# Optimization experiments

Measured on AMD Instinct MI355X. Metric: run time of the kernel, lower is better.

Reference implementation:

```python
import jax, jax.numpy as jnp
import numpy as np

B, C_IN, C_OUT, H, MAXN = 128, 32, 32, 4096, 6


def setup_inputs() -> dict:
    key = jax.random.key(0)
    ks = jax.random.split(key, 6)
    x = jax.random.normal(ks[0], (B, C_IN, H), dtype=jnp.float32)
    weight = jax.random.normal(ks[1], (C_OUT, C_IN, MAXN + 1), dtype=jnp.float32) * 0.05
    bias = jax.random.normal(ks[2], (C_OUT,), dtype=jnp.float32) * 0.05
    gamma = jnp.ones((C_OUT,), dtype=jnp.float32)
    beta = jnp.zeros((C_OUT,), dtype=jnp.float32)
    # hex neighbor table; -1 marks invalid (boundary) neighbors
    neighbors = jax.random.randint(ks[3], (H, MAXN), -1, H, dtype=jnp.int64)
    return {"x": x, "weight": weight, "bias": bias, "gamma": gamma,
            "beta": beta, "neighbors": neighbors, "groups": 1}


def reference(x, weight, bias, gamma, beta, neighbors, groups):
    Bsz, Cin, Hn = x.shape
    Cout, _, K = weight.shape  # K = total_inputs = max_neighbors + 1
    G = groups
    # global std normalization (torch std: unbiased, ddof=1)
    x = x / (jnp.std(x, ddof=1) + 1e-5)
    valid = (neighbors >= 0)                      # [H, K-1]
    idx = jnp.clip(neighbors, 0, None)
    nbr = x[:, :, idx] * valid.astype(x.dtype)[None, None]   # [B,C,H,K-1]
    allv = jnp.concatenate([x[..., None], nbr], axis=3)      # [B,C,H,K]
    allv = allv.reshape(Bsz, G, Cin // G, Hn, K)
    w = weight.reshape(G, Cout // G, Cin // G, K)
    out = jnp.einsum('bgihk,goik->bgoh', allv, w).reshape(Bsz, Cout, Hn)
    total_valid = valid.sum(axis=1).astype(out.dtype)[None, None] + 1.0  # [1,1,H]
    out = out / (total_valid + 1e-6)
    out = out + bias[None, :, None]
    # BatchNorm1d in training mode: per-channel over (batch, hex), biased var
    mean = out.mean(axis=(0, 2), keepdims=True)
    var = out.var(axis=(0, 2), keepdims=True)
    out = gamma[None, :, None] * (out - mean) * jax.lax.rsqrt(var + 1e-5) + beta[None, :, None]
    return out
```

## Files before the change

### kernel.cpp

```cpp
#include <hip/hip_runtime.h>
#include <stdint.h>
#include <stddef.h>

#define BSZ 128
#define CIN 32
#define COUT 32
#define HN 4096
#define K7 7
#define NTOT (BSZ*CIN*HN)
#define NBH  (BSZ*HN)

typedef __attribute__((ext_vector_type(8))) short short8;
typedef __attribute__((ext_vector_type(4))) float f32x4;

#define WS_OB   0
#define WS_WT   33554432
#define WS_NBR  33568768
#define WS_INVD 33699840
#define WS_OSTP 33716224
#define WS_OST  33781760

__device__ __forceinline__ unsigned short f32_to_bf16(float f){
    union { float f; uint32_t u; } v; v.f = f;
    uint32_t u = v.u;
    return (unsigned short)((u + 0x7FFFu + ((u >> 16) & 1u)) >> 16);
}
__device__ __forceinline__ float bf16_to_f32(unsigned short h){
    union { uint32_t u; float f; } v; v.u = ((uint32_t)h) << 16;
    return v.f;
}

__global__ void kinit(const int* __restrict__ nbr,
                      const float* __restrict__ w,
                      int* __restrict__ nbr_pack,
                      float* __restrict__ invd,
                      unsigned short* __restrict__ wt,
                      float* __restrict__ ostatp){
    int t = threadIdx.x;
    if (blockIdx.x < 16){
        int h = blockIdx.x*256 + t;
        #pragma unroll
        for (int j = 0; j < 4; j++) ostatp[h*4 + j] = 0.0f;
        int cnt = 0;
        int pk[8];
        #pragma unroll
        for (int j = 0; j < 6; j++){
            int iv = nbr[h*6 + j];
            if (iv >= HN) iv = HN - 1;
            if (iv >= 0) cnt++; else iv = -1;
            pk[j] = iv;
        }
        pk[6] = cnt; pk[7] = 0;
        #pragma unroll
        for (int j = 0; j < 8; j++) nbr_pack[h*8 + j] = pk[j];
        invd[h] = 1.0f / ((float)cnt + 1.0f + 1e-6f);
    } else {
        for (int i = t; i < COUT*K7*CIN; i += 256){
            int o  = i / (K7*CIN);
            int kk = (i / CIN) % K7;
            int c  = i % CIN;
            wt[i] = f32_to_bf16(w[(o*CIN + c)*K7 + kk]);
        }
    }
}

__global__ void ktrans(const float* __restrict__ x,
                       unsigned short* __restrict__ xt){
    __shared__ float tile[32][260];
    int b  = blockIdx.x >> 4;
    int h0 = (blockIdx.x & 15) << 8;
    int t  = threadIdx.x;
    #pragma unroll
    for (int l = 0; l < 8; l++){
        int linear = l*256 + t;
        int c  = linear >> 6;
        int h4 = linear & 63;
        float4 v = *(const float4*)(x + ((size_t)(b*CIN + c))*HN + h0 + h4*4);
        *(float4*)&tile[c][h4*4] = v;
    }
    __syncthreads();
    int cg = (t & 3) * 8;
    int hw = t >> 2;
    #pragma unroll
    for (int r = 0; r < 4; r++){
        int h = r*64 + hw;
        alignas(16) unsigned short tmp[8];
        #pragma unroll
        for (int j = 0; j < 8; j++) tmp[j] = f32_to_bf16(tile[cg + j][h]);
        *(uint4*)(xt + ((size_t)(b*HN + h0 + h))*32 + cg) = *(const uint4*)tmp;
    }
}

__global__ __launch_bounds__(256) void kconv(
    const unsigned short* __restrict__ xt,
    const unsigned short* __restrict__ wt,
    const int* __restrict__ nbrp,
    const float* __restrict__ invd,
    unsigned short* __restrict__ ob,
    float* __restrict__ ostatp)
{
    int lane = threadIdx.x & 63;
    int wv   = threadIdx.x >> 6;
    int n    = lane & 15;
    int quad = lane >> 4;
    int xcd  = blockIdx.x & 7;
    int j    = blockIdx.x >> 3;
    int b    = xcd*16 + (j >> 4);
    int hbase= ((j & 15)*4 + wv) * 64;

    short8 af[2][K7];
    #pragma unroll
    for (int mt = 0; mt < 2; mt++){
        int o = n + 16*mt;
        #pragma unroll
        for (int kk = 0; kk < K7; kk++)
            af[mt][kk] = *(const short8*)(wt + (size_t)(o*K7 + kk)*CIN + quad*8);
    }

    float sacc[8]  = {0,0,0,0,0,0,0,0};
    float sacc2[8] = {0,0,0,0,0,0,0,0};
    const short8 zero8 = {0,0,0,0,0,0,0,0};
    const unsigned short* xb = xt + (size_t)b*HN*CIN;

    int h = hbase + n;
    int4 na = *(const int4*)(nbrp + h*8);
    int4 nb = *(const int4*)(nbrp + h*8 + 4);
    float idv = invd[h];

    #pragma unroll 1
    for (int it = 0; it < 4; it++){
        int hc = hbase + it*16 + n;
        int hn = hbase + (it < 3 ? it+1 : it)*16 + n;
        int4 na2 = *(const int4*)(nbrp + hn*8);
        int4 nb2 = *(const int4*)(nbrp + hn*8 + 4);
        float idv2 = invd[hn];

        short8 bfr[K7];
        bfr[0] = *(const short8*)(xb + (size_t)hc*CIN + quad*8);
        int rows[6] = {na.x, na.y, na.z, na.w, nb.x, nb.y};
        #pragma unroll
        for (int kk = 0; kk < 6; kk++){
            int row  = rows[kk];
            int rowc = row < 0 ? 0 : row;
            bfr[kk+1] = *(const short8*)(xb + (size_t)rowc*CIN + quad*8);
            if (row < 0) bfr[kk+1] = zero8;
        }
        f32x4 acc0 = {0.f,0.f,0.f,0.f};
        f32x4 acc1 = {0.f,0.f,0.f,0.f};
        #pragma unroll
        for (int kk = 0; kk < K7; kk++){
            acc0 = __builtin_amdgcn_mfma_f32_16x16x32_bf16(af[0][kk], bfr[kk], acc0, 0, 0, 0);
            acc1 = __builtin_amdgcn_mfma_f32_16x16x32_bf16(af[1][kk], bfr[kk], acc1, 0, 0, 0);
        }
        #pragma unroll
        for (int mt = 0; mt < 2; mt++){
            f32x4 a = mt ? acc1 : acc0;
            #pragma unroll
            for (int r = 0; r < 4; r++){
                int o = mt*16 + quad*4 + r;
                float v = a[r]*idv;
                ob[((size_t)(b*COUT + o))*HN + hc] = f32_to_bf16(v);
                sacc[mt*4 + r]  += v;
                sacc2[mt*4 + r] += v*v;
            }
        }
        na = na2; nb = nb2; idv = idv2;
    }
    #pragma unroll
    for (int bit = 1; bit < 16; bit <<= 1){
        #pragma unroll
        for (int i = 0; i < 8; i++){
            sacc[i]  += __shfl_xor(sacc[i],  bit);
            sacc2[i] += __shfl_xor(sacc2[i], bit);
        }
    }
    if (n == 0){
        int slot = blockIdx.x & 255;
        #pragma unroll
        for (int mt = 0; mt < 2; mt++)
            #pragma unroll
            for (int r = 0; r < 4; r++){
                int o = mt*16 + quad*4 + r;
                atomicAdd(&ostatp[slot*64 + o],      sacc[mt*4 + r]);
                atomicAdd(&ostatp[slot*64 + 32 + o], sacc2[mt*4 + r]);
            }
    }
}

__global__ void kred(const float* __restrict__ ostatp,
                     float* __restrict__ ostat){
    __shared__ float part[4][64];
    int t = threadIdx.x;
    int a = t & 63;
    int g = t >> 6;
    float s = 0.0f;
    #pragma unroll
    for (int j = 0; j < 64; j++)
        s += ostatp[(g*64 + j)*64 + a];
    part[g][a] = s;
    __syncthreads();
    if (t < 64)
        ostat[t] = part[0][t] + part[1][t] + part[2][t] + part[3][t];
}

__global__ void kbn(const unsigned short* __restrict__ ob,
                    float* __restrict__ out,
                    const float* __restrict__ ostat,
                    const float* __restrict__ gamma,
                    const float* __restrict__ beta){
    __shared__ float sc[32], sh[32];
    int t = threadIdx.x;
    if (t < 32){
        float mean = ostat[t] * (1.0f/(float)NBH);
        float var  = ostat[32 + t] * (1.0f/(float)NBH) - mean*mean;
        float s = gamma[t] * rsqrtf(var + 1e-5f);
        sc[t] = s;
        sh[t] = beta[t] - mean*s;
    }
    __syncthreads();
    int gid    = blockIdx.x*blockDim.x + t;
    int stride = gridDim.x*blockDim.x;
    for (int i = gid; i < NTOT/8; i += stride){
        int o = (i >> 9) & 31;
        uint4 raw = ((const uint4*)ob)[i];
        const unsigned short* p = (const unsigned short*)&raw;
        float s = sc[o], bsh = sh[o];
        float4 r0, r1;
        r0.x = bf16_to_f32(p[0])*s + bsh;
        r0.y = bf16_to_f32(p[1])*s + bsh;
        r0.z = bf16_to_f32(p[2])*s + bsh;
        r0.w = bf16_to_f32(p[3])*s + bsh;
        r1.x = bf16_to_f32(p[4])*s + bsh;
        r1.y = bf16_to_f32(p[5])*s + bsh;
        r1.z = bf16_to_f32(p[6])*s + bsh;
        r1.w = bf16_to_f32(p[7])*s + bsh;
        ((float4*)out)[i*2]     = r0;
        ((float4*)out)[i*2 + 1] = r1;
    }
}

extern "C" void kernel_launch(void* const* d_in, const int* in_sizes, int n_in,
                              void* d_out, int out_size, void* d_ws, size_t ws_size,
                              hipStream_t stream) {
    const float* x      = (const float*)d_in[0];
    const float* weight = (const float*)d_in[1];
    const float* gamma  = (const float*)d_in[3];
    const float* beta   = (const float*)d_in[4];
    const int*   nbr    = (const int*)d_in[5];

    char* ws = (char*)d_ws;
    unsigned short* ob    = (unsigned short*)(ws + WS_OB);
    unsigned short* wt    = (unsigned short*)(ws + WS_WT);
    int*            nbrp  = (int*)(ws + WS_NBR);
    float*          invd  = (float*)(ws + WS_INVD);
    float*          ostatp= (float*)(ws + WS_OSTP);
    float*          ostat = (float*)(ws + WS_OST);
    float*          out   = (float*)d_out;
    unsigned short* xt    = (unsigned short*)d_out + 16777216;

    kinit <<<17,   256, 0, stream>>>(nbr, weight, nbrp, invd, wt, ostatp);
    ktrans<<<2048, 256, 0, stream>>>(x, xt);
    kconv <<<2048, 256, 0, stream>>>(xt, wt, nbrp, invd, ob, ostatp);
    kred  <<<1,    256, 0, stream>>>(ostatp, ostat);
    kbn   <<<2048, 256, 0, stream>>>(ob, out, ostat, gamma, beta);
}
```

Measured before the change: 184.9 us.

## Recompute convolution in second pass to fuse BatchNorm apply and drop intermediate

Replaces the bf16 intermediate buffer and separate BN-apply kernel with a templated conv kernel run twice: once to accumulate channel statistics, once to recompute the conv and write normalized fp32 output directly. Also double-buffers the neighbor gathers and fully unrolls the hex loop to overlap loads with MFMA work. This trades extra conv compute and an extra read of the transposed input for removing the intermediate write/read, at the cost of higher register usage.

```diff
diff --git a/kernel.cpp b/kernel.cpp
--- a/kernel.cpp
+++ b/kernel.cpp
@@ -13,7 +13,7 @@
 typedef __attribute__((ext_vector_type(8))) short short8;
 typedef __attribute__((ext_vector_type(4))) float f32x4;
 
-#define WS_OB   0
+#define WS_XT   0
 #define WS_WT   33554432
 #define WS_NBR  33568768
 #define WS_INVD 33699840
@@ -24,10 +24,6 @@
     union { float f; uint32_t u; } v; v.f = f;
     uint32_t u = v.u;
     return (unsigned short)((u + 0x7FFFu + ((u >> 16) & 1u)) >> 16);
-}
-__device__ __forceinline__ float bf16_to_f32(unsigned short h){
-    union { uint32_t u; float f; } v; v.u = ((uint32_t)h) << 16;
-    return v.f;
 }
 
 __global__ void kinit(const int* __restrict__ nbr,
@@ -91,12 +87,30 @@
     }
 }
 
-__global__ __launch_bounds__(256) void kconv(
+__device__ __forceinline__ void gather7(short8* dst, const unsigned short* xb,
+                                        int selfrow, int4 na, int4 nb, int quad){
+    const short8 zero8 = {0,0,0,0,0,0,0,0};
+    dst[0] = *(const short8*)(xb + (size_t)selfrow*CIN + quad*8);
+    int rows[6] = {na.x, na.y, na.z, na.w, nb.x, nb.y};
+    #pragma unroll
+    for (int k = 0; k < 6; k++){
+        int r  = rows[k];
+        int rc = r < 0 ? 0 : r;
+        dst[k+1] = *(const short8*)(xb + (size_t)rc*CIN + quad*8);
+        if (r < 0) dst[k+1] = zero8;
+    }
+}
+
+template<bool APPLY>
+__global__ __launch_bounds__(256) void kconv_t(
     const unsigned short* __restrict__ xt,
     const unsigned short* __restrict__ wt,
     const int* __restrict__ nbrp,
     const float* __restrict__ invd,
-    unsigned short* __restrict__ ob,
+    const float* __restrict__ ostat,
+    const float* __restrict__ gamma,
+    const float* __restrict__ beta,
+    float* __restrict__ out,
     float* __restrict__ ostatp)
 {
     int lane = threadIdx.x & 63;
@@ -117,73 +131,92 @@
             af[mt][kk] = *(const short8*)(wt + (size_t)(o*K7 + kk)*CIN + quad*8);
     }
 
+    float sc8[2][4], sh8[2][4];
+    if (APPLY){
+        #pragma unroll
+        for (int mt = 0; mt < 2; mt++)
+            #pragma unroll
+            for (int r = 0; r < 4; r++){
+                int o = mt*16 + quad*4 + r;
+                float mean = ostat[o]      * (1.0f/(float)NBH);
+                float var  = ostat[32 + o] * (1.0f/(float)NBH) - mean*mean;
+                float s = gamma[o] * rsqrtf(var + 1e-5f);
+                sc8[mt][r] = s;
+                sh8[mt][r] = beta[o] - mean*s;
+            }
+    }
+
     float sacc[8]  = {0,0,0,0,0,0,0,0};
     float sacc2[8] = {0,0,0,0,0,0,0,0};
-    const short8 zero8 = {0,0,0,0,0,0,0,0};
     const unsigned short* xb = xt + (size_t)b*HN*CIN;
-
-    int h = hbase + n;
-    int4 na = *(const int4*)(nbrp + h*8);
-    int4 nb = *(const int4*)(nbrp + h*8 + 4);
-    float idv = invd[h];
-
-    #pragma unroll 1
+    int hn0 = hbase + n;
+
+    int4 na[2], nb[2]; float iv[2];
+    short8 buf[2][K7];
+    na[0] = *(const int4*)(nbrp + hn0*8);
+    nb[0] = *(const int4*)(nbrp + hn0*8 + 4);
+    iv[0] = invd[hn0];
+    na[1] = *(const int4*)(nbrp + (hn0+16)*8);
+    nb[1] = *(const int4*)(nbrp + (hn0+16)*8 + 4);
+    iv[1] = invd[hn0+16];
+    gather7(buf[0], xb, hn0, na[0], nb[0], quad);
+
+    #pragma unroll
     for (int it = 0; it < 4; it++){
-        int hc = hbase + it*16 + n;
-        int hn = hbase + (it < 3 ? it+1 : it)*16 + n;
-        int4 na2 = *(const int4*)(nbrp + hn*8);
-        int4 nb2 = *(const int4*)(nbrp + hn*8 + 4);
-        float idv2 = invd[hn];
-
-        short8 bfr[K7];
-        bfr[0] = *(const short8*)(xb + (size_t)hc*CIN + quad*8);
-        int rows[6] = {na.x, na.y, na.z, na.w, nb.x, nb.y};
-        #pragma unroll
-        for (int kk = 0; kk < 6; kk++){
-            int row  = rows[kk];
-            int rowc = row < 0 ? 0 : row;
-            bfr[kk+1] = *(const short8*)(xb + (size_t)rowc*CIN + quad*8);
-            if (row < 0) bfr[kk+1] = zero8;
+        int s = it & 1, o2 = s ^ 1;
+        float idv = iv[s];
+        if (it + 1 < 4)
+            gather7(buf[o2], xb, hn0 + (it+1)*16, na[o2], nb[o2], quad);
+        if (it + 2 < 4){
+            na[s] = *(const int4*)(nbrp + (hn0 + (it+2)*16)*8);
+            nb[s] = *(const int4*)(nbrp + (hn0 + (it+2)*16)*8 + 4);
+            iv[s] = invd[hn0 + (it+2)*16];
         }
         f32x4 acc0 = {0.f,0.f,0.f,0.f};
         f32x4 acc1 = {0.f,0.f,0.f,0.f};
         #pragma unroll
         for (int kk = 0; kk < K7; kk++){
-            acc0 = __builtin_amdgcn_mfma_f32_16x16x32_bf16(af[0][kk], bfr[kk], acc0, 0, 0, 0);
-            acc1 = __builtin_amdgcn_mfma_f32_16x16x32_bf16(af[1][kk], bfr[kk], acc1, 0, 0, 0);
-        }
+            acc0 = __builtin_amdgcn_mfma_f32_16x16x32_bf16(af[0][kk], buf[s][kk], acc0, 0, 0, 0);
+            acc1 = __builtin_amdgcn_mfma_f32_16x16x32_bf16(af[1][kk], buf[s][kk], acc1, 0, 0, 0);
+        }
+        int hc = hbase + it*16 + n;
         #pragma unroll
         for (int mt = 0; mt < 2; mt++){
             f32x4 a = mt ? acc1 : acc0;
             #pragma unroll
             for (int r = 0; r < 4; r++){
-                int o = mt*16 + quad*4 + r;
                 float v = a[r]*idv;
-                ob[((size_t)(b*COUT + o))*HN + hc] = f32_to_bf16(v);
-                sacc[mt*4 + r]  += v;
-                sacc2[mt*4 + r] += v*v;
+                if (APPLY){
+                    int o = mt*16 + quad*4 + r;
+                    out[((size_t)(b*COUT + o))*HN + hc] = v*sc8[mt][r] + sh8[mt][r];
+                } else {
+                    sacc[mt*4 + r]  += v;
+                    sacc2[mt*4 + r] += v*v;
+                }
             }
         }
-        na = na2; nb = nb2; idv = idv2;
-    }
-    #pragma unroll
-    for (int bit = 1; bit < 16; bit <<= 1){
-        #pragma unroll
-        for (int i = 0; i < 8; i++){
-            sacc[i]  += __shfl_xor(sacc[i],  bit);
-            sacc2[i] += __shfl_xor(sacc2[i], bit);
-        }
-    }
-    if (n == 0){
-        int slot = blockIdx.x & 255;
-        #pragma unroll
-        for (int mt = 0; mt < 2; mt++)
-            #pragma unroll
-            for (int r = 0; r < 4; r++){
-                int o = mt*16 + quad*4 + r;
-                atomicAdd(&ostatp[slot*64 + o],      sacc[mt*4 + r]);
-                atomicAdd(&ostatp[slot*64 + 32 + o], sacc2[mt*4 + r]);
+    }
+
+    if (!APPLY){
+        #pragma unroll
+        for (int bit = 1; bit < 16; bit <<= 1){
+            #pragma unroll
+            for (int i = 0; i < 8; i++){
+                sacc[i]  += __shfl_xor(sacc[i],  bit);
+                sacc2[i] += __shfl_xor(sacc2[i], bit);
             }
+        }
+        if (n == 0){
+            int slot = blockIdx.x & 255;
+            #pragma unroll
+            for (int mt = 0; mt < 2; mt++)
+                #pragma unroll
+                for (int r = 0; r < 4; r++){
+                    int o = mt*16 + quad*4 + r;
+                    atomicAdd(&ostatp[slot*64 + o],      sacc[mt*4 + r]);
+                    atomicAdd(&ostatp[slot*64 + 32 + o], sacc2[mt*4 + r]);
+                }
+        }
     }
 }
 
@@ -201,42 +234,6 @@
     __syncthreads();
     if (t < 64)
         ostat[t] = part[0][t] + part[1][t] + part[2][t] + part[3][t];
-}
-
-__global__ void kbn(const unsigned short* __restrict__ ob,
-                    float* __restrict__ out,
-                    const float* __restrict__ ostat,
-                    const float* __restrict__ gamma,
-                    const float* __restrict__ beta){
-    __shared__ float sc[32], sh[32];
-    int t = threadIdx.x;
-    if (t < 32){
-        float mean = ostat[t] * (1.0f/(float)NBH);
-        float var  = ostat[32 + t] * (1.0f/(float)NBH) - mean*mean;
-        float s = gamma[t] * rsqrtf(var + 1e-5f);
-        sc[t] = s;
-        sh[t] = beta[t] - mean*s;
-    }
-    __syncthreads();
-    int gid    = blockIdx.x*blockDim.x + t;
-    int stride = gridDim.x*blockDim.x;
-    for (int i = gid; i < NTOT/8; i += stride){
-        int o = (i >> 9) & 31;
-        uint4 raw = ((const uint4*)ob)[i];
-        const unsigned short* p = (const unsigned short*)&raw;
-        float s = sc[o], bsh = sh[o];
-        float4 r0, r1;
-        r0.x = bf16_to_f32(p[0])*s + bsh;
-        r0.y = bf16_to_f32(p[1])*s + bsh;
-        r0.z = bf16_to_f32(p[2])*s + bsh;
-        r0.w = bf16_to_f32(p[3])*s + bsh;
-        r1.x = bf16_to_f32(p[4])*s + bsh;
-        r1.y = bf16_to_f32(p[5])*s + bsh;
-        r1.z = bf16_to_f32(p[6])*s + bsh;
-        r1.w = bf16_to_f32(p[7])*s + bsh;
-        ((float4*)out)[i*2]     = r0;
-        ((float4*)out)[i*2 + 1] = r1;
-    }
 }
 
 extern "C" void kernel_launch(void* const* d_in, const int* in_sizes, int n_in,
@@ -249,18 +246,17 @@
     const int*   nbr    = (const int*)d_in[5];
 
     char* ws = (char*)d_ws;
-    unsigned short* ob    = (unsigned short*)(ws + WS_OB);
+    unsigned short* xt    = (unsigned short*)(ws + WS_XT);
     unsigned short* wt    = (unsigned short*)(ws + WS_WT);
     int*            nbrp  = (int*)(ws + WS_NBR);
     float*          invd  = (float*)(ws + WS_INVD);
     float*          ostatp= (float*)(ws + WS_OSTP);
     float*          ostat = (float*)(ws + WS_OST);
     float*          out   = (float*)d_out;
-    unsigned short* xt    = (unsigned short*)d_out + 16777216;
-
-    kinit <<<17,   256, 0, stream>>>(nbr, weight, nbrp, invd, wt, ostatp);
-    ktrans<<<2048, 256, 0, stream>>>(x, xt);
-    kconv <<<2048, 256, 0, stream>>>(xt, wt, nbrp, invd, ob, ostatp);
-    kred  <<<1,    256, 0, stream>>>(ostatp, ostat);
-    kbn   <<<2048, 256, 0, stream>>>(ob, out, ostat, gamma, beta);
-}
+
+    kinit        <<<17,   256, 0, stream>>>(nbr, weight, nbrp, invd, wt, ostatp);
+    ktrans       <<<2048, 256, 0, stream>>>(x, xt);
+    kconv_t<false><<<2048, 256, 0, stream>>>(xt, wt, nbrp, invd, nullptr, nullptr, nullptr, nullptr, ostatp);
+    kred         <<<1,    256, 0, stream>>>(ostatp, ostat);
+    kconv_t<true> <<<2048, 256, 0, stream>>>(xt, wt, nbrp, invd, ostat, gamma, beta, out, nullptr);
+}
```

New measurement: 191.2 us. 3.4% more time.
